# Kernel tuning notes

Hardware: AMD Instinct MI355X
Metric: run time of the kernel (lower is better)

## Reference

```python
import jax, jax.numpy as jnp
import numpy as np

B, S, D, H, DFF = 4, 2048, 1024, 16, 4096
DK = D // H
EPS = 1e-5


def setup_inputs() -> dict:
    key = jax.random.key(0)
    ks = jax.random.split(key, 10)
    s = 0.02
    return {
        "x": jax.random.normal(ks[0], (B, S, D), jnp.float32),
        "wq": jax.random.normal(ks[1], (D, D), jnp.float32) * s,
        "wk": jax.random.normal(ks[2], (D, D), jnp.float32) * s,
        "wv": jax.random.normal(ks[3], (D, D), jnp.float32) * s,
        "wo": jax.random.normal(ks[4], (D, D), jnp.float32) * s,
        "w1": jax.random.normal(ks[5], (D, DFF), jnp.float32) * s,
        "b1": jnp.zeros((DFF,), jnp.float32),
        "w2": jax.random.normal(ks[6], (DFF, D), jnp.float32) * s,
        "b2": jnp.zeros((D,), jnp.float32),
        "g1": jnp.ones((D,), jnp.float32),
        "be1": jnp.zeros((D,), jnp.float32),
        "g2": jnp.ones((D,), jnp.float32),
        "be2": jnp.zeros((D,), jnp.float32),
    }


def _layernorm(x, g, b):
    mu = jnp.mean(x, axis=-1, keepdims=True)
    var = jnp.mean(jnp.square(x - mu), axis=-1, keepdims=True)
    return (x - mu) * jax.lax.rsqrt(var + EPS) * g + b


def reference(x, wq, wk, wv, wo, w1, b1, w2, b2, g1, be1, g2, be2):
    # --- self-attention block (pre-LN) ---
    residual = x
    h = _layernorm(x, g1, be1)
    q = (h @ wq).reshape(B, S, H, DK).transpose(0, 2, 1, 3)  # [B,H,S,DK]
    k = (h @ wk).reshape(B, S, H, DK).transpose(0, 2, 1, 3)
    v = (h @ wv).reshape(B, S, H, DK).transpose(0, 2, 1, 3)
    scores = jnp.einsum("bhqd,bhkd->bhqk", q, k) / jnp.sqrt(jnp.float32(DK))
    weights = jax.nn.softmax(scores, axis=-1)
    weights = jnp.nan_to_num(weights, nan=0.0)
    attn = jnp.einsum("bhqk,bhkd->bhqd", weights, v)
    attn = attn.transpose(0, 2, 1, 3).reshape(B, S, D)
    x = residual + attn @ wo
    # --- FFN block (pre-LN) ---
    residual = x
    h = _layernorm(x, g2, be2)
    h = jax.nn.relu(h @ w1 + b1) @ w2 + b2
    return residual + h
```

## Files before the change

### kernel.cpp

```cpp
#include <hip/hip_runtime.h>
#include <stdint.h>

#define B_ 4
#define S_ 2048
#define D_ 1024
#define H_ 16
#define DFF_ 4096
#define QSTR 3072

typedef __attribute__((ext_vector_type(8))) short short8;
typedef __attribute__((ext_vector_type(4))) short short4v;
typedef __attribute__((ext_vector_type(4))) float floatx4;
typedef __attribute__((ext_vector_type(16))) float floatx16;

typedef const __attribute__((address_space(1))) void* gas_ptr;
typedef __attribute__((address_space(3))) void* las_ptr;

__device__ __forceinline__ short f2bf(float f) {
  union { float f; uint32_t u; } v; v.f = f;
  uint32_t r = v.u + 0x7fffu + ((v.u >> 16) & 1u);
  return (short)(r >> 16);
}

__global__ __launch_bounds__(256) void ln_kernel(
    const float* __restrict__ x, const float* __restrict__ g,
    const float* __restrict__ be, short* __restrict__ out)
{
  const int row = blockIdx.x;
  const int tid = threadIdx.x;
  const float4 v = ((const float4*)(x + (size_t)row * D_))[tid];
  float s1 = v.x + v.y + v.z + v.w;
  float s2 = v.x*v.x + v.y*v.y + v.z*v.z + v.w*v.w;
#pragma unroll
  for (int off = 1; off < 64; off <<= 1) {
    s1 += __shfl_xor(s1, off);
    s2 += __shfl_xor(s2, off);
  }
  __shared__ float r1[4], r2[4];
  if ((tid & 63) == 0) { r1[tid >> 6] = s1; r2[tid >> 6] = s2; }
  __syncthreads();
  s1 = r1[0] + r1[1] + r1[2] + r1[3];
  s2 = r2[0] + r2[1] + r2[2] + r2[3];
  const float mu = s1 * (1.0f / D_);
  const float var = s2 * (1.0f / D_) - mu * mu;
  const float rs = rsqrtf(var + 1e-5f);
  const float4 gv = ((const float4*)g)[tid];
  const float4 bv = ((const float4*)be)[tid];
  short4v o;
  o.x = f2bf((v.x - mu) * rs * gv.x + bv.x);
  o.y = f2bf((v.y - mu) * rs * gv.y + bv.y);
  o.z = f2bf((v.z - mu) * rs * gv.z + bv.z);
  o.w = f2bf((v.w - mu) * rs * gv.w + bv.w);
  *(short4v*)&out[(size_t)row * D_ + tid * 4] = o;
}

__global__ __launch_bounds__(256) void transpose_all(
    const float* __restrict__ wq, const float* __restrict__ wk,
    const float* __restrict__ wv, const float* __restrict__ wo,
    const float* __restrict__ w1, const float* __restrict__ w2,
    short* __restrict__ wqkvT, short* __restrict__ woT,
    short* __restrict__ w1T, short* __restrict__ w2T)
{
  const uint32_t pid = blockIdx.x;
  const float* in; short* out;
  int R, C, tile, xsh;
  if (pid < 4096) {
    const int which = pid >> 10; tile = pid & 1023;
    R = 1024; C = 1024; xsh = 5;
    in  = (which == 0) ? wq : (which == 1) ? wk : (which == 2) ? wv : wo;
    out = (which == 3) ? woT : wqkvT + (size_t)which * 1024 * 1024;
  } else if (pid < 8192) {
    tile = pid - 4096; R = 1024; C = 4096; xsh = 7; in = w1; out = w1T;
  } else {
    tile = pid - 8192; R = 4096; C = 1024; xsh = 5; in = w2; out = w2T;
  }
  const int c0 = (tile & ((1 << xsh) - 1)) * 32;
  const int r0 = (tile >> xsh) * 32;

  __shared__ float t[32][33];
  const int tx = threadIdx.x & 31, ty = threadIdx.x >> 5;
#pragma unroll
  for (int i = 0; i < 4; i++)
    t[ty + i * 8][tx] = in[(size_t)(r0 + ty + i * 8) * C + c0 + tx];
  __syncthreads();
#pragma unroll
  for (int i = 0; i < 4; i++)
    out[(size_t)(c0 + ty + i * 8) * R + r0 + tx] = f2bf(t[tx][ty + i * 8]);
}

__global__ __launch_bounds__(256, 4) void gemm_bt(
    const short* __restrict__ A, const short* __restrict__ Bt,
    float* __restrict__ outf, short* __restrict__ outb,
    short* __restrict__ outbK, short* __restrict__ vtT,
    const float* __restrict__ bias, const float* __restrict__ resid,
    int M, int N, int K, int do_relu, int split, int group)
{
  __shared__ short As[2 * 128 * 32];
  __shared__ short Bs[2 * 128 * 32];
  const int tid = threadIdx.x;
  const int wave = tid >> 6;
  const int lane = tid & 63;
  const int quad = lane >> 4;
  const int l16 = lane & 15;

  const uint32_t nblk = gridDim.x;
  const uint32_t pid = blockIdx.y * nblk + blockIdx.x;
  const uint32_t nig = (uint32_t)group * nblk;
  const uint32_t gid = pid / nig;
  const uint32_t within = pid - gid * nig;
  const uint32_t bm = gid * group + within % group;
  const uint32_t bn = within / group;
  const int tm = bm * 128;
  const int tn = bn * 128;

  const int wm = (wave & 1) * 64;
  const int wn = (wave >> 1) * 64;
  const int srow = lane >> 2;
  const int scol = (lane & 3) * 8;

  floatx4 acc[4][4];
#pragma unroll
  for (int i = 0; i < 4; i++)
#pragma unroll
    for (int j = 0; j < 4; j++) acc[i][j] = floatx4{0.f, 0.f, 0.f, 0.f};

  const short* gA0 = A + (size_t)(tm + wave * 32 + srow) * K + scol;
  const short* gB0 = Bt + (size_t)(tn + wave * 32 + srow) * K + scol;

  for (int kt = 0; kt < K; kt += 64) {
    __syncthreads();
    __builtin_amdgcn_global_load_lds((gas_ptr)(gA0 + kt),                      (las_ptr)(&As[wave * 1024]),        16, 0, 0);
    __builtin_amdgcn_global_load_lds((gas_ptr)(gA0 + kt + (size_t)16 * K),     (las_ptr)(&As[wave * 1024 + 512]),  16, 0, 0);
    __builtin_amdgcn_global_load_lds((gas_ptr)(gB0 + kt),                      (las_ptr)(&Bs[wave * 1024]),        16, 0, 0);
    __builtin_amdgcn_global_load_lds((gas_ptr)(gB0 + kt + (size_t)16 * K),     (las_ptr)(&Bs[wave * 1024 + 512]),  16, 0, 0);
    __builtin_amdgcn_global_load_lds((gas_ptr)(gA0 + kt + 32),                 (las_ptr)(&As[4096 + wave * 1024]),       16, 0, 0);
    __builtin_amdgcn_global_load_lds((gas_ptr)(gA0 + kt + 32 + (size_t)16 * K),(las_ptr)(&As[4096 + wave * 1024 + 512]), 16, 0, 0);
    __builtin_amdgcn_global_load_lds((gas_ptr)(gB0 + kt + 32),                 (las_ptr)(&Bs[4096 + wave * 1024]),       16, 0, 0);
    __builtin_amdgcn_global_load_lds((gas_ptr)(gB0 + kt + 32 + (size_t)16 * K),(las_ptr)(&Bs[4096 + wave * 1024 + 512]), 16, 0, 0);
    __syncthreads();

#pragma unroll
    for (int ksub = 0; ksub < 2; ksub++) {
      const int hb = ksub * 4096;
      short8 af[4], bfv[4];
#pragma unroll
      for (int mi = 0; mi < 4; mi++)
        af[mi] = *(const short8*)&As[hb + (wm + mi * 16 + l16) * 32 + quad * 8];
#pragma unroll
      for (int ni = 0; ni < 4; ni++)
        bfv[ni] = *(const short8*)&Bs[hb + (wn + ni * 16 + l16) * 32 + quad * 8];
#pragma unroll
      for (int mi = 0; mi < 4; mi++)
#pragma unroll
        for (int ni = 0; ni < 4; ni++)
          acc[mi][ni] = __builtin_amdgcn_mfma_f32_16x16x32_bf16(af[mi], bfv[ni], acc[mi][ni], 0, 0, 0);
    }
  }

  short* ob = outb;
  int Nst = N;
  int cbase = tn;
  int vpart = 0;
  if (split) {
    const int part = tn >> 10;
    if (part == 2) vpart = 1;
    else ob = (part == 0) ? outb : outbK;
    Nst = D_;
    cbase = tn & (D_ - 1);
  }

  if (vpart) {
#pragma unroll
    for (int mi = 0; mi < 4; mi++) {
      const int row0 = tm + wm + mi * 16 + quad * 4;
      const int bb = row0 >> 11, s0r = row0 & 2047;
#pragma unroll
      for (int ni = 0; ni < 4; ni++) {
        const int cst = cbase + wn + ni * 16 + l16;
        short4v o;
#pragma unroll
        for (int r = 0; r < 4; r++) o[r] = f2bf(acc[mi][ni][r]);
        *(short4v*)&vtT[((size_t)(bb << 10) + cst) * (size_t)S_ + s0r] = o;
      }
    }
    return;
  }

#pragma unroll
  for (int mi = 0; mi < 4; mi++) {
    const int row0 = tm + wm + mi * 16 + quad * 4;
#pragma unroll
    for (int ni = 0; ni < 4; ni++) {
      const int col = tn + wn + ni * 16 + l16;
      const int cst = cbase + wn + ni * 16 + l16;
      const float bv = bias ? bias[col] : 0.0f;
#pragma unroll
      for (int r = 0; r < 4; r++) {
        const size_t idx = (size_t)(row0 + r) * Nst + cst;
        float v = acc[mi][ni][r] + bv;
        if (do_relu) v = fmaxf(v, 0.0f);
        if (resid) v += resid[idx];
        if (outf) outf[idx] = v;
        if (ob) ob[idx] = f2bf(v);
      }
    }
  }
}

__global__ __launch_bounds__(256, 4) void gemm_bt_n64(
    const short* __restrict__ A, const short* __restrict__ Bt,
    float* __restrict__ outf,
    const float* __restrict__ bias, const float* __restrict__ resid,
    int M, int N, int K, int group)
{
  __shared__ short As[2 * 128 * 32];
  __shared__ short Bs[2 * 64 * 32];
  const int tid = threadIdx.x;
  const int wave = tid >> 6;
  const int lane = tid & 63;
  const int quad = lane >> 4;
  const int l16 = lane & 15;

  const uint32_t nblk = gridDim.x;
  const uint32_t pid = blockIdx.y * nblk + blockIdx.x;
  const uint32_t nig = (uint32_t)group * nblk;
  const uint32_t gid = pid / nig;
  const uint32_t within = pid - gid * nig;
  const uint32_t bm = gid * group + within % group;
  const uint32_t bn = within / group;
  const int tm = bm * 128;
  const int tn = bn * 64;

  const int wm = (wave & 1) * 64;
  const int wn = (wave >> 1) * 32;
  const int srow = lane >> 2;
  const int scol = (lane & 3) * 8;

  floatx4 acc[4][2];
#pragma unroll
  for (int i = 0; i < 4; i++)
#pragma unroll
    for (int j = 0; j < 2; j++) acc[i][j] = floatx4{0.f, 0.f, 0.f, 0.f};

  const short* gA0 = A + (size_t)(tm + wave * 32 + srow) * K + scol;
  const short* gB0 = Bt + (size_t)(tn + wave * 16 + srow) * K + scol;

  for (int kt = 0; kt < K; kt += 64) {
    __syncthreads();
    __builtin_amdgcn_global_load_lds((gas_ptr)(gA0 + kt),                      (las_ptr)(&As[wave * 1024]),        16, 0, 0);
    __builtin_amdgcn_global_load_lds((gas_ptr)(gA0 + kt + (size_t)16 * K),     (las_ptr)(&As[wave * 1024 + 512]),  16, 0, 0);
    __builtin_amdgcn_global_load_lds((gas_ptr)(gA0 + kt + 32),                 (las_ptr)(&As[4096 + wave * 1024]),       16, 0, 0);
    __builtin_amdgcn_global_load_lds((gas_ptr)(gA0 + kt + 32 + (size_t)16 * K),(las_ptr)(&As[4096 + wave * 1024 + 512]), 16, 0, 0);
    __builtin_amdgcn_global_load_lds((gas_ptr)(gB0 + kt),      (las_ptr)(&Bs[wave * 512]),        16, 0, 0);
    __builtin_amdgcn_global_load_lds((gas_ptr)(gB0 + kt + 32), (las_ptr)(&Bs[2048 + wave * 512]), 16, 0, 0);
    __syncthreads();

#pragma unroll
    for (int ksub = 0; ksub < 2; ksub++) {
      const int ha = ksub * 4096;
      const int hbv = ksub * 2048;
      short8 af[4], bfv[2];
#pragma unroll
      for (int mi = 0; mi < 4; mi++)
        af[mi] = *(const short8*)&As[ha + (wm + mi * 16 + l16) * 32 + quad * 8];
#pragma unroll
      for (int ni = 0; ni < 2; ni++)
        bfv[ni] = *(const short8*)&Bs[hbv + (wn + ni * 16 + l16) * 32 + quad * 8];
#pragma unroll
      for (int mi = 0; mi < 4; mi++)
#pragma unroll
        for (int ni = 0; ni < 2; ni++)
          acc[mi][ni] = __builtin_amdgcn_mfma_f32_16x16x32_bf16(af[mi], bfv[ni], acc[mi][ni], 0, 0, 0);
    }
  }

#pragma unroll
  for (int mi = 0; mi < 4; mi++) {
    const int row0 = tm + wm + mi * 16 + quad * 4;
#pragma unroll
    for (int ni = 0; ni < 2; ni++) {
      const int col = tn + wn + ni * 16 + l16;
      const float bv = bias ? bias[col] : 0.0f;
#pragma unroll
      for (int r = 0; r < 4; r++) {
        const size_t idx = (size_t)(row0 + r) * N + col;
        float v = acc[mi][ni][r] + bv;
        if (resid) v += resid[idx];
        outf[idx] = v;
      }
    }
  }
}

__device__ __forceinline__ int kvidx(int row, int scol) {
  return (row << 6) + (scol ^ ((row & 7) << 3));
}

__global__ __launch_bounds__(256, 4) void attn_kernel(
    const short* __restrict__ qb, const short* __restrict__ kb,
    const short* __restrict__ vtb, short* __restrict__ attb)
{
  __shared__ short Ks[2][64 * 64];
  __shared__ short Vts[2][64 * 64];
  __shared__ float lbuf[4][32];

  const int tid = threadIdx.x;
  const int wave = tid >> 6, lane = tid & 63;
  const int l31 = lane & 31, hi = lane >> 5;
  const int qt = blockIdx.x, bh = blockIdx.y;
  const int b = bh >> 4, h = bh & 15;
  const size_t rowbase = (size_t)b * S_;
  const int hcol = h * 64;
  const int r = tid >> 2, c = (tid & 3) * 16;

  short8 qf[4];
  {
    const short* gq = qb + (rowbase + qt * 128 + wave * 32 + l31) * D_ + hcol + hi * 8;
#pragma unroll
    for (int st = 0; st < 4; st++) {
      short8 t = *(const short8*)(gq + st * 16);
#pragma unroll
      for (int i = 0; i < 8; i++) {
        const float f = __uint_as_float(((uint32_t)(uint16_t)t[i]) << 16) * 0.18033688f;
        t[i] = (short)((__float_as_uint(f) + 0x8000u) >> 16);
      }
      qf[st] = t;
    }
  }

  floatx16 Of[2];
#pragma unroll
  for (int nd = 0; nd < 2; nd++)
#pragma unroll
    for (int i = 0; i < 16; i++) Of[nd][i] = 0.f;
  float lrun = 0.f;

  const short* gk0 = kb + (rowbase + r) * D_ + hcol + c;
  const short* gv0 = vtb + ((size_t)bh * 64 + r) * S_ + c;

  short8 kr0 = *(const short8*)gk0, kr1 = *(const short8*)(gk0 + 8);
  short8 vr0 = *(const short8*)gv0, vr1 = *(const short8*)(gv0 + 8);
  *(short8*)&Ks[0][kvidx(r, c)]      = kr0;
  *(short8*)&Ks[0][kvidx(r, c + 8)]  = kr1;
  *(short8*)&Vts[0][kvidx(r, c)]     = vr0;
  *(short8*)&Vts[0][kvidx(r, c + 8)] = vr1;

  for (int kt = 0; kt < S_; kt += 64) {
    const int cur = (kt >> 6) & 1;
    const bool more = (kt + 64 < S_);
    if (more) {
      const short* gk = gk0 + (size_t)(kt + 64) * D_;
      const short* gv = gv0 + (kt + 64);
      kr0 = *(const short8*)gk; kr1 = *(const short8*)(gk + 8);
      vr0 = *(const short8*)gv; vr1 = *(const short8*)(gv + 8);
    }
    __syncthreads();

#pragma unroll
    for (int sub = 0; sub < 2; sub++) {
      floatx16 s;
#pragma unroll
      for (int i = 0; i < 16; i++) s[i] = 0.f;
#pragma unroll
      for (int st = 0; st < 4; st++) {
        const short8 kf = *(const short8*)&Ks[cur][kvidx(sub * 32 + l31, st * 16 + hi * 8)];
        s = __builtin_amdgcn_mfma_f32_32x32x16_bf16(kf, qf[st], s, 0, 0, 0);
      }
      float p[16];
#pragma unroll
      for (int i = 0; i < 16; i++) { p[i] = __builtin_amdgcn_exp2f(s[i]); lrun += p[i]; }
      short8 pf[2];
#pragma unroll
      for (int kw = 0; kw < 2; kw++) {
        const int o = kw * 8;
        uint32_t wa, wb, wc, wd;
        asm("v_cvt_pk_bf16_f32 %0, %1, %2" : "=v"(wa) : "v"(p[o + 0]), "v"(p[o + 1]));
        asm("v_cvt_pk_bf16_f32 %0, %1, %2" : "=v"(wb) : "v"(p[o + 4]), "v"(p[o + 5]));
        asm("v_cvt_pk_bf16_f32 %0, %1, %2" : "=v"(wc) : "v"(p[o + 2]), "v"(p[o + 3]));
        asm("v_cvt_pk_bf16_f32 %0, %1, %2" : "=v"(wd) : "v"(p[o + 6]), "v"(p[o + 7]));
        asm("v_permlane32_swap_b32 %0, %1" : "+v"(wa), "+v"(wb));
        asm("v_permlane32_swap_b32 %0, %1" : "+v"(wc), "+v"(wd));
        union { uint32_t u[4]; short8 s8; } pk;
        pk.u[0] = wa; pk.u[1] = wc; pk.u[2] = wb; pk.u[3] = wd;
        pf[kw] = pk.s8;
      }
#pragma unroll
      for (int kw = 0; kw < 2; kw++)
#pragma unroll
        for (int nd = 0; nd < 2; nd++) {
          const short8 vf = *(const short8*)&Vts[cur][kvidx(nd * 32 + l31, sub * 32 + kw * 16 + hi * 8)];
          Of[nd] = __builtin_amdgcn_mfma_f32_32x32x16_bf16(pf[kw], vf, Of[nd], 0, 0, 0);
        }
    }

    if (more) {
      const int nxt = cur ^ 1;
      *(short8*)&Ks[nxt][kvidx(r, c)]      = kr0;
      *(short8*)&Ks[nxt][kvidx(r, c + 8)]  = kr1;
      *(short8*)&Vts[nxt][kvidx(r, c)]     = vr0;
      *(short8*)&Vts[nxt][kvidx(r, c + 8)] = vr1;
    }
  }

  const float ltot = lrun + __shfl_xor(lrun, 32);
  if (hi == 0) lbuf[wave][l31] = ltot;
  asm volatile("" ::: "memory");
#pragma unroll
  for (int reg = 0; reg < 16; reg++) {
    const int q = (reg & 3) + 4 * hi + 8 * (reg >> 2);
    const float inv = 1.0f / lbuf[wave][q];
    const size_t base = (rowbase + qt * 128 + wave * 32 + q) * D_ + hcol + l31;
    attb[base]      = f2bf(Of[0][reg] * inv);
    attb[base + 32] = f2bf(Of[1][reg] * inv);
  }
}

extern "C" void kernel_launch(void* const* d_in, const int* in_sizes, int n_in,
                              void* d_out, int out_size, void* d_ws, size_t ws_size,
                              hipStream_t stream) {
  const float* x   = (const float*)d_in[0];
  const float* wq  = (const float*)d_in[1];
  const float* wk  = (const float*)d_in[2];
  const float* wv  = (const float*)d_in[3];
  const float* wo  = (const float*)d_in[4];
  const float* w1  = (const float*)d_in[5];
  const float* b1  = (const float*)d_in[6];
  const float* w2  = (const float*)d_in[7];
  const float* b2  = (const float*)d_in[8];
  const float* g1  = (const float*)d_in[9];
  const float* be1 = (const float*)d_in[10];
  const float* g2  = (const float*)d_in[11];
  const float* be2 = (const float*)d_in[12];
  float* out = (float*)d_out;

  const size_t MROWS = (size_t)B_ * S_;
  char* p = (char*)d_ws;
  auto take = [&](size_t bytes) { char* r = p; p += (bytes + 255) & ~(size_t)255; return r; };
  short* hb    = (short*)take(MROWS * D_ * 2);
  short* h2b   = (short*)take(MROWS * D_ * 2);
  short* qbuf  = (short*)take(MROWS * D_ * 2);
  short* kbuf  = (short*)take(MROWS * D_ * 2);
  short* vtb   = (short*)take(MROWS * D_ * 2);
  short* attb  = (short*)take(MROWS * D_ * 2);
  short* ffb   = (short*)take(MROWS * DFF_ * 2);
  short* wqkvT = (short*)take((size_t)3 * D_ * D_ * 2);
  short* woT   = (short*)take((size_t)D_ * D_ * 2);
  short* w1T   = (short*)take((size_t)D_ * DFF_ * 2);
  short* w2T   = (short*)take((size_t)DFF_ * D_ * 2);
  float* x1    = (float*)take(MROWS * D_ * 4);

  transpose_all<<<12288, 256, 0, stream>>>(wq, wk, wv, wo, w1, w2,
                                           wqkvT, woT, w1T, w2T);

  ln_kernel<<<MROWS, 256, 0, stream>>>(x, g1, be1, hb);

  gemm_bt<<<dim3(QSTR / 128, MROWS / 128), 256, 0, stream>>>(
      hb, wqkvT, nullptr, qbuf, kbuf, vtb, nullptr, nullptr, MROWS, QSTR, D_, 0, 1, 8);

  attn_kernel<<<dim3(S_ / 128, B_ * H_), 256, 0, stream>>>(qbuf, kbuf, vtb, attb);

  gemm_bt_n64<<<dim3(D_ / 64, MROWS / 128), 256, 0, stream>>>(
      attb, woT, x1, nullptr, x, MROWS, D_, D_, 8);

  ln_kernel<<<MROWS, 256, 0, stream>>>(x1, g2, be2, h2b);

  gemm_bt<<<dim3(DFF_ / 128, MROWS / 128), 256, 0, stream>>>(
      h2b, w1T, nullptr, ffb, nullptr, nullptr, b1, nullptr, MROWS, DFF_, D_, 1, 0, 8);

  gemm_bt_n64<<<dim3(D_ / 64, MROWS / 128), 256, 0, stream>>>(
      ffb, w2T, out, b2, x1, MROWS, D_, DFF_, 4);

  (void)in_sizes; (void)n_in; (void)out_size; (void)ws_size;
}
```

Before: 547.0 us.

## Stream attention K/V tiles directly into LDS with global_load_lds and swizzle

Replaces the register-staged K/V prefetch (global load to VGPRs, then ds_write after compute) with direct global-to-LDS DMA loads issued right after the barrier into the other buffer. The LDS swizzle changes to an XOR that also uses row bits 3-4, and each lane's source column is pre-permuted to match it. The change also adds s_setprio around the MFMA sections and splits the row-sum accumulator in two to shorten the dependency chain. This removes the staging VGPRs and the LDS write instructions. It relies on the permuted source addressing matching the read-side swizzle.

```diff
diff --git a/kernel.cpp b/kernel.cpp
--- a/kernel.cpp
+++ b/kernel.cpp
@@ -292,8 +292,11 @@
   }
 }
 
+__device__ __forceinline__ int swz64(int row) {
+  return (row & 7) ^ ((row >> 3) & 3);
+}
 __device__ __forceinline__ int kvidx(int row, int scol) {
-  return (row << 6) + (scol ^ ((row & 7) << 3));
+  return (row << 6) + (scol ^ (swz64(row) << 3));
 }
 
 __global__ __launch_bounds__(256, 4) void attn_kernel(
@@ -311,7 +314,11 @@
   const int b = bh >> 4, h = bh & 15;
   const size_t rowbase = (size_t)b * S_;
   const int hcol = h * 64;
-  const int r = tid >> 2, c = (tid & 3) * 16;
+
+  const int lr = lane >> 3, lg = lane & 7;
+  const int sgran = (lg ^ lr ^ wave) * 8;
+  const short* ksrc = kb + (rowbase + wave * 8 + lr) * D_ + hcol + sgran;
+  const short* vsrc = vtb + ((size_t)bh * 64 + wave * 8 + lr) * S_ + sgran;
 
   short8 qf[4];
   {
@@ -333,42 +340,45 @@
   for (int nd = 0; nd < 2; nd++)
 #pragma unroll
     for (int i = 0; i < 16; i++) Of[nd][i] = 0.f;
-  float lrun = 0.f;
-
-  const short* gk0 = kb + (rowbase + r) * D_ + hcol + c;
-  const short* gv0 = vtb + ((size_t)bh * 64 + r) * S_ + c;
-
-  short8 kr0 = *(const short8*)gk0, kr1 = *(const short8*)(gk0 + 8);
-  short8 vr0 = *(const short8*)gv0, vr1 = *(const short8*)(gv0 + 8);
-  *(short8*)&Ks[0][kvidx(r, c)]      = kr0;
-  *(short8*)&Ks[0][kvidx(r, c + 8)]  = kr1;
-  *(short8*)&Vts[0][kvidx(r, c)]     = vr0;
-  *(short8*)&Vts[0][kvidx(r, c + 8)] = vr1;
+  float lrun0 = 0.f, lrun1 = 0.f;
+
+  __builtin_amdgcn_global_load_lds((gas_ptr)ksrc,                      (las_ptr)(&Ks[0][(wave * 8) * 64]),        16, 0, 0);
+  __builtin_amdgcn_global_load_lds((gas_ptr)(ksrc + (size_t)32 * D_),  (las_ptr)(&Ks[0][(32 + wave * 8) * 64]),   16, 0, 0);
+  __builtin_amdgcn_global_load_lds((gas_ptr)vsrc,                      (las_ptr)(&Vts[0][(wave * 8) * 64]),       16, 0, 0);
+  __builtin_amdgcn_global_load_lds((gas_ptr)(vsrc + (size_t)32 * S_),  (las_ptr)(&Vts[0][(32 + wave * 8) * 64]),  16, 0, 0);
 
   for (int kt = 0; kt < S_; kt += 64) {
     const int cur = (kt >> 6) & 1;
-    const bool more = (kt + 64 < S_);
-    if (more) {
-      const short* gk = gk0 + (size_t)(kt + 64) * D_;
-      const short* gv = gv0 + (kt + 64);
-      kr0 = *(const short8*)gk; kr1 = *(const short8*)(gk + 8);
-      vr0 = *(const short8*)gv; vr1 = *(const short8*)(gv + 8);
-    }
     __syncthreads();
+
+    if (kt + 64 < S_) {
+      const int nxt = cur ^ 1;
+      const short* kp = ksrc + (size_t)(kt + 64) * D_;
+      const short* vp = vsrc + (kt + 64);
+      __builtin_amdgcn_global_load_lds((gas_ptr)kp,                      (las_ptr)(&Ks[nxt][(wave * 8) * 64]),        16, 0, 0);
+      __builtin_amdgcn_global_load_lds((gas_ptr)(kp + (size_t)32 * D_),  (las_ptr)(&Ks[nxt][(32 + wave * 8) * 64]),   16, 0, 0);
+      __builtin_amdgcn_global_load_lds((gas_ptr)vp,                      (las_ptr)(&Vts[nxt][(wave * 8) * 64]),       16, 0, 0);
+      __builtin_amdgcn_global_load_lds((gas_ptr)(vp + (size_t)32 * S_),  (las_ptr)(&Vts[nxt][(32 + wave * 8) * 64]),  16, 0, 0);
+    }
 
 #pragma unroll
     for (int sub = 0; sub < 2; sub++) {
       floatx16 s;
 #pragma unroll
       for (int i = 0; i < 16; i++) s[i] = 0.f;
+      __builtin_amdgcn_s_setprio(1);
 #pragma unroll
       for (int st = 0; st < 4; st++) {
         const short8 kf = *(const short8*)&Ks[cur][kvidx(sub * 32 + l31, st * 16 + hi * 8)];
         s = __builtin_amdgcn_mfma_f32_32x32x16_bf16(kf, qf[st], s, 0, 0, 0);
       }
+      __builtin_amdgcn_s_setprio(0);
       float p[16];
 #pragma unroll
-      for (int i = 0; i < 16; i++) { p[i] = __builtin_amdgcn_exp2f(s[i]); lrun += p[i]; }
+      for (int i = 0; i < 16; i++) {
+        p[i] = __builtin_amdgcn_exp2f(s[i]);
+        if (i & 1) lrun1 += p[i]; else lrun0 += p[i];
+      }
       short8 pf[2];
 #pragma unroll
       for (int kw = 0; kw < 2; kw++) {
@@ -384,6 +394,7 @@
         pk.u[0] = wa; pk.u[1] = wc; pk.u[2] = wb; pk.u[3] = wd;
         pf[kw] = pk.s8;
       }
+      __builtin_amdgcn_s_setprio(1);
 #pragma unroll
       for (int kw = 0; kw < 2; kw++)
 #pragma unroll
@@ -391,17 +402,11 @@
           const short8 vf = *(const short8*)&Vts[cur][kvidx(nd * 32 + l31, sub * 32 + kw * 16 + hi * 8)];
           Of[nd] = __builtin_amdgcn_mfma_f32_32x32x16_bf16(pf[kw], vf, Of[nd], 0, 0, 0);
         }
-    }
-
-    if (more) {
-      const int nxt = cur ^ 1;
-      *(short8*)&Ks[nxt][kvidx(r, c)]      = kr0;
-      *(short8*)&Ks[nxt][kvidx(r, c + 8)]  = kr1;
-      *(short8*)&Vts[nxt][kvidx(r, c)]     = vr0;
-      *(short8*)&Vts[nxt][kvidx(r, c + 8)] = vr1;
-    }
-  }
-
+      __builtin_amdgcn_s_setprio(0);
+    }
+  }
+
+  const float lrun = lrun0 + lrun1;
   const float ltot = lrun + __shfl_xor(lrun, 32);
   if (hi == 0) lbuf[wave][l31] = ltot;
   asm volatile("" ::: "memory");
```

New measurement: 525.4 us. 1.04x faster.
